# Kernel tuning notes

Measured on AMD Instinct MI355X. Metric: run time of the kernel, lower is better.

The kernel has to match this reference:

```python
import jax, jax.numpy as jnp
import numpy as np

HIDDEN = 64
NUM_FEATURES = 32
BATCH = 64
SEQ = 2048


def setup_inputs() -> dict:
    key = jax.random.key(0)
    k_t, k_m, k_wr, k_br, k_wi, k_bi = jax.random.split(key, 6)
    # strictly increasing event times via cumsum of positive gaps
    gaps = jax.random.uniform(k_t, (BATCH, SEQ), minval=0.01, maxval=1.0)
    times = jnp.cumsum(gaps, axis=1)  # [B, T]
    marks = jax.random.uniform(k_m, (BATCH, SEQ, NUM_FEATURES))
    batch = jnp.concatenate([times[:, :, None], marks], axis=2)  # [B, T, 1+F]
    d_in = NUM_FEATURES + HIDDEN
    W_rec = jax.random.normal(k_wr, (d_in, 7 * HIDDEN)) / jnp.sqrt(d_in)
    b_rec = jnp.zeros((7 * HIDDEN,))
    W_int = jax.random.normal(k_wi, (HIDDEN, NUM_FEATURES)) / jnp.sqrt(HIDDEN)
    b_int = jnp.zeros((NUM_FEATURES,))
    return {"batch": batch, "W_rec": W_rec, "b_rec": b_rec,
            "W_int": W_int, "b_int": b_int}


def _ctlstm_forward(batch, W_rec, b_rec, W_int, b_int):
    times = batch[:, :, 0]          # [B, T]
    marks = batch[:, :, 1:]         # [B, T, F]
    B, T, _ = marks.shape
    # inter-event time for step t is times[t+1]-times[t]; last step has no decay
    dt = jnp.diff(times, axis=1)                                   # [B, T-1]
    dt = jnp.concatenate([dt, jnp.zeros((B, 1), dt.dtype)], 1)     # [B, T]

    def step(carry, inputs):
        h, c_decay, c_bar = carry
        x_t, dt_t = inputs          # [B, F], [B]
        z = jnp.concatenate([x_t, h], axis=1) @ W_rec + b_rec      # [B, 7H]
        i, f, g, o, i_bar, f_bar, delta = jnp.split(z, 7, axis=1)
        i = jax.nn.sigmoid(i)
        f = jax.nn.sigmoid(f)
        g = jnp.tanh(g)
        o = jax.nn.sigmoid(o)
        i_bar = jax.nn.sigmoid(i_bar)
        f_bar = jax.nn.sigmoid(f_bar)
        delta = jax.nn.softplus(delta)
        c = f * c_decay + i * g                    # (5a)
        c_bar_n = f_bar * c_bar + i_bar * g        # (5b)
        c_decay_n = c_bar_n + (c - c_bar_n) * jnp.exp(-delta * dt_t[:, None])  # (7)
        h_n = o * jnp.tanh(c_decay_n)              # (4b)
        intensity = jax.nn.softplus(h_n @ W_int + b_int)  # (4a)
        return (h_n, c_decay_n, c_bar_n), (o, c, c_bar_n, delta, intensity)

    h0 = jnp.zeros((B, HIDDEN), batch.dtype)
    carry0 = (h0, h0, h0)
    xs = (jnp.swapaxes(marks, 0, 1), jnp.swapaxes(dt, 0, 1))  # time-major
    _, (o, c, c_bar, delta, intensity) = jax.lax.scan(step, carry0, xs)
    tm = lambda a: jnp.swapaxes(a, 0, 1)  # [T,B,*] -> [B,T,*]
    # intensity defined only for t < T-1 (last decay step is skipped in original)
    return (tm(o), tm(c), tm(c_bar), tm(delta), tm(intensity)[:, :-1, :])


def reference(batch, W_rec, b_rec, W_int, b_int):
    return _ctlstm_forward(batch, W_rec, b_rec, W_int, b_int)
```

## Files before the change

### kernel.cpp

```cpp
#include <hip/hip_runtime.h>
#include <hip/hip_bf16.h>

#define BATCHN 64
#define SEQ    2048
#define HID    64
#define NF     32
#define DIN    96
#define G7     448
#define CH     33
#define REC_T  256

using bf16 = __hip_bfloat16;

__device__ __forceinline__ float b2f(bf16 v) { return __bfloat162float(v); }

__device__ __forceinline__ float ldin(const void* p, size_t i, bool f32) {
    return f32 ? ((const float*)p)[i] : b2f(((const bf16*)p)[i]);
}

__device__ __forceinline__ float fast_rcp(float x) { return __builtin_amdgcn_rcpf(x); }
__device__ __forceinline__ float sigmoid_f(float x) {
    return fast_rcp(1.0f + __expf(-x));
}
__device__ __forceinline__ float tanh_f(float x) {
    float e = __expf(2.0f * x);
    return 1.0f - 2.0f * fast_rcp(e + 1.0f);
}
__device__ __forceinline__ float softplus_f(float x) {
    float e = __expf(-fabsf(x));
    return fmaxf(x, 0.0f) + __logf(1.0f + e);
}

__device__ __forceinline__ float rl(float v, int lane) {
    return __uint_as_float(__builtin_amdgcn_readlane(__float_as_uint(v), lane));
}

__global__ void detect_dtype(const void* batch, int* flag) {
    if (threadIdx.x != 0 || blockIdx.x != 0) return;
    const float* bf = (const float*)batch;
    bool mono = true;
    float prev = bf[0];
    if (!(prev > 0.004f && prev < 1.3f)) mono = false;
    for (int t = 1; t < 16 && mono; ++t) {
        float cur = bf[(size_t)t * CH];
        if (!(cur > prev && (cur - prev) < 1.3f)) mono = false;
        prev = cur;
    }
    *flag = mono ? 1 : 0;
}

__global__ __launch_bounds__(G7) void xproj_gemm(
    const void* __restrict__ batch, const void* __restrict__ W_rec,
    const void* __restrict__ b_rec, float* __restrict__ xz,
    const int* __restrict__ flag)
{
    const bool f32 = *flag != 0;
    const int tid = threadIdx.x;
    const size_t base = (size_t)blockIdx.x * 64;

    float wx[NF];
    if (f32) {
        const float* W = (const float*)W_rec;
#pragma unroll
        for (int k = 0; k < NF; ++k) wx[k] = W[(size_t)k * G7 + tid];
    } else {
        const bf16* W = (const bf16*)W_rec;
#pragma unroll
        for (int k = 0; k < NF; ++k) wx[k] = b2f(W[(size_t)k * G7 + tid]);
    }
    const float bias = ldin(b_rec, tid, f32);

    __shared__ __align__(16) float s_x[64][NF];
    for (int i = tid; i < 64 * NF; i += G7) {
        const int r = i >> 5, k = i & 31;
        s_x[r][k] = ldin(batch, (base + r) * CH + 1 + k, f32);
    }
    __syncthreads();

    for (int r = 0; r < 64; ++r) {
        const float4* xv = (const float4*)s_x[r];
        float a0 = 0.f, a1 = 0.f, a2 = 0.f, a3 = 0.f;
#pragma unroll
        for (int k4 = 0; k4 < NF / 4; ++k4) {
            float4 v = xv[k4];
            a0 = fmaf(v.x, wx[4 * k4 + 0], a0);
            a1 = fmaf(v.y, wx[4 * k4 + 1], a1);
            a2 = fmaf(v.z, wx[4 * k4 + 2], a2);
            a3 = fmaf(v.w, wx[4 * k4 + 3], a3);
        }
        xz[(base + r) * G7 + tid] = bias + ((a0 + a1) + (a2 + a3));
    }
}

__global__ __launch_bounds__(REC_T, 1) void ctlstm_rec_xz4(
    const void* __restrict__ batch, const void* __restrict__ W_rec,
    const float* __restrict__ xz, float* __restrict__ out,
    float* __restrict__ h_ws, const int* __restrict__ flag)
{
    const bool f32 = *flag != 0;
    const int tid  = threadIdx.x;
    const int wave = tid >> 6;
    const int lane = tid & 63;
    const int b    = blockIdx.x;
    const size_t bT = (size_t)b * SEQ;

    float* out_o  = out;
    float* out_c  = out + (size_t)BATCHN * SEQ * HID;
    float* out_cb = out + 2 * (size_t)BATCHN * SEQ * HID;
    float* out_dl = out + 3 * (size_t)BATCHN * SEQ * HID;

    __shared__ float s_act[2][G7];
    __shared__ float s_times[SEQ];

    const int c0 = tid;
    const int c1 = (wave < 3) ? tid + 256 : tid;

    float2 wh[HID];
    if (f32) {
        const float* W = (const float*)W_rec;
#pragma unroll
        for (int k = 0; k < HID; ++k) {
            wh[k].x = W[(size_t)(NF + k) * G7 + c0];
            wh[k].y = W[(size_t)(NF + k) * G7 + c1];
        }
    } else {
        const bf16* W = (const bf16*)W_rec;
#pragma unroll
        for (int k = 0; k < HID; ++k) {
            wh[k].x = b2f(W[(size_t)(NF + k) * G7 + c0]);
            wh[k].y = b2f(W[(size_t)(NF + k) * G7 + c1]);
        }
    }

    for (int i = tid; i < SEQ; i += REC_T)
        s_times[i] = ldin(batch, (bT + i) * CH, f32);

    float h_reg = 0.0f, c_decay = 0.0f, c_bar = 0.0f;

    float xa0 = xz[bT * G7 + c0];
    float xb0 = xz[bT * G7 + c1];
    float xa1 = xz[(bT + 1) * G7 + c0];
    float xb1 = xz[(bT + 1) * G7 + c1];
    __syncthreads();

    for (int t = 0; t < SEQ; ++t) {
        float xa2 = 0.0f, xb2 = 0.0f;
        if (t + 2 < SEQ) {
            xa2 = xz[(bT + t + 2) * G7 + c0];
            xb2 = xz[(bT + t + 2) * G7 + c1];
        }

        float a0x = 0.f, a1x = 0.f, a2x = 0.f, a3x = 0.f;
        float a0y = 0.f, a1y = 0.f, a2y = 0.f, a3y = 0.f;
#pragma unroll
        for (int k = 0; k < HID; k += 4) {
            const float h0 = rl(h_reg, k + 0);
            const float h1 = rl(h_reg, k + 1);
            const float h2 = rl(h_reg, k + 2);
            const float h3 = rl(h_reg, k + 3);
            a0x = fmaf(h0, wh[k + 0].x, a0x); a0y = fmaf(h0, wh[k + 0].y, a0y);
            a1x = fmaf(h1, wh[k + 1].x, a1x); a1y = fmaf(h1, wh[k + 1].y, a1y);
            a2x = fmaf(h2, wh[k + 2].x, a2x); a2y = fmaf(h2, wh[k + 2].y, a2y);
            a3x = fmaf(h3, wh[k + 3].x, a3x); a3y = fmaf(h3, wh[k + 3].y, a3y);
        }
        const float z0 = xa0 + ((a0x + a1x) + (a2x + a3x));
        const float z1 = xb0 + ((a0y + a1y) + (a2y + a3y));

        const float act0 = (wave == 2) ? tanh_f(z0) : sigmoid_f(z0);
        const float act1 = (wave == 2) ? softplus_f(z1) : sigmoid_f(z1);

        const int p = t & 1;
        s_act[p][c0] = act0;
        if (wave < 3) s_act[p][c1] = act1;

        asm volatile("s_waitcnt lgkmcnt(0)" ::: "memory");
        __builtin_amdgcn_s_barrier();
        __builtin_amdgcn_sched_barrier(0);

        const float ig = s_act[p][lane];
        const float fg = s_act[p][HID + lane];
        const float gg = s_act[p][2 * HID + lane];
        const float og = s_act[p][3 * HID + lane];
        const float ib = s_act[p][4 * HID + lane];
        const float fb = s_act[p][5 * HID + lane];
        const float dl = s_act[p][6 * HID + lane];
        const float c   = fg * c_decay + ig * gg;
        const float cbn = fb * c_bar + ib * gg;
        float dt = (t + 1 < SEQ) ? (s_times[t + 1] - s_times[t]) : 0.0f;
        dt = fmaxf(dt, 0.0f);
        const float cd = cbn + (c - cbn) * __expf(-dl * dt);
        const float h  = og * tanh_f(cd);
        c_decay = cd;
        c_bar   = cbn;
        h_reg   = h;

        const size_t idx = (bT + t) * HID + lane;
        if (wave == 0)      out_c[idx]  = c;
        else if (wave == 1) out_cb[idx] = cbn;
        else if (wave == 2) h_ws[idx]   = h;
        else                { out_o[idx] = og; out_dl[idx] = dl; }

        xa0 = xa1; xb0 = xb1; xa1 = xa2; xb1 = xb2;
    }
}

__global__ __launch_bounds__(G7, 2) void ctlstm_rec(
    const void* __restrict__ batch, const void* __restrict__ W_rec,
    const void* __restrict__ b_rec, float* __restrict__ out,
    float* __restrict__ h_ws, int use_ws, const int* __restrict__ flag)
{
    const bool f32 = flag ? (*flag != 0) : true;
    const int tid = threadIdx.x;
    const int b   = blockIdx.x;
    const size_t bT = (size_t)b * SEQ;

    float* out_o  = out;
    float* out_c  = out + (size_t)BATCHN * SEQ * HID;
    float* out_cb = out + 2 * (size_t)BATCHN * SEQ * HID;
    float* out_dl = out + 3 * (size_t)BATCHN * SEQ * HID;

    __shared__ __align__(16) float s_in[DIN];
    __shared__ float s_act[G7];
    __shared__ float s_times[SEQ];

    float wcol[DIN];
    if (f32) {
        const float* W = (const float*)W_rec;
#pragma unroll
        for (int k = 0; k < DIN; ++k) wcol[k] = W[(size_t)k * G7 + tid];
    } else {
        const bf16* W = (const bf16*)W_rec;
#pragma unroll
        for (int k = 0; k < DIN; ++k) wcol[k] = b2f(W[(size_t)k * G7 + tid]);
    }
    const float bias = ldin(b_rec, tid, f32);

    for (int i = tid; i < SEQ; i += G7)
        s_times[i] = ldin(batch, (bT + i) * CH, f32);

    if (tid >= NF && tid < DIN) s_in[tid] = 0.0f;
    float c_decay = 0.0f, c_bar = 0.0f;

    float xpref = 0.0f;
    if (tid < NF) xpref = ldin(batch, bT * CH + 1 + tid, f32);
    __syncthreads();

    const int gate = tid >> 6;
    const int lane = tid & 63;

    for (int t = 0; t < SEQ; ++t) {
        if (tid < NF) s_in[tid] = xpref;
        __syncthreads();

        const float4* sv = (const float4*)s_in;
        float a0 = 0.f, a1 = 0.f, a2 = 0.f, a3 = 0.f;
#pragma unroll
        for (int k4 = 0; k4 < DIN / 4; ++k4) {
            float4 v = sv[k4];
            a0 = fmaf(v.x, wcol[4 * k4 + 0], a0);
            a1 = fmaf(v.y, wcol[4 * k4 + 1], a1);
            a2 = fmaf(v.z, wcol[4 * k4 + 2], a2);
            a3 = fmaf(v.w, wcol[4 * k4 + 3], a3);
        }
        const float z = bias + ((a0 + a1) + (a2 + a3));

        float act;
        if (gate == 2)      act = tanh_f(z);
        else if (gate == 6) act = softplus_f(z);
        else                act = sigmoid_f(z);
        s_act[tid] = act;

        const size_t oidx = (bT + t) * HID + lane;
        if (gate == 3) out_o[oidx]  = act;
        if (gate == 6) out_dl[oidx] = act;
        __syncthreads();

        if (tid < HID) {
            const float ig = s_act[tid];
            const float fg = s_act[HID + tid];
            const float gg = s_act[2 * HID + tid];
            const float og = s_act[3 * HID + tid];
            const float ib = s_act[4 * HID + tid];
            const float fb = s_act[5 * HID + tid];
            const float dl = s_act[6 * HID + tid];
            const float c  = fg * c_decay + ig * gg;
            const float cb = fb * c_bar + ib * gg;
            float dt = (t + 1 < SEQ) ? (s_times[t + 1] - s_times[t]) : 0.0f;
            dt = fmaxf(dt, 0.0f);
            const float cd = cb + (c - cb) * __expf(-dl * dt);
            const float h  = og * tanh_f(cd);
            c_decay = cd;
            c_bar   = cb;
            s_in[NF + tid] = h;
            const size_t idx = (bT + t) * HID + tid;
            out_c[idx]  = c;
            out_cb[idx] = cb;
            if (use_ws) h_ws[idx] = h;
        }
        if (tid < NF && t + 1 < SEQ)
            xpref = ldin(batch, (bT + t + 1) * CH + 1 + tid, f32);
    }
}

__global__ __launch_bounds__(256) void intensity_ws(
    const float* __restrict__ h_ws, const void* __restrict__ W_int,
    const void* __restrict__ b_int, float* __restrict__ out_int,
    const int* __restrict__ flag)
{
    const bool f32 = flag ? (*flag != 0) : true;
    __shared__ float s_w[HID * NF];
    __shared__ float s_b[NF];
    const int tx = threadIdx.x, ty = threadIdx.y;
    const int lt = ty * 32 + tx;
    for (int k = lt; k < HID * NF; k += 256) s_w[k] = ldin(W_int, k, f32);
    if (lt < NF) s_b[lt] = ldin(b_int, lt, f32);
    __syncthreads();

    const int b = blockIdx.y;
    const int t = blockIdx.x * 8 + ty;
    if (t >= SEQ - 1) return;
    const float* hr = h_ws + ((size_t)b * SEQ + t) * HID;
    float acc = s_b[tx];
#pragma unroll
    for (int k = 0; k < HID; ++k) acc = fmaf(hr[k], s_w[k * NF + tx], acc);
    out_int[((size_t)b * (SEQ - 1) + t) * NF + tx] = softplus_f(acc);
}

__global__ __launch_bounds__(256) void intensity_rec(
    const void* __restrict__ batch, const float* __restrict__ out,
    const void* __restrict__ W_int, const void* __restrict__ b_int,
    float* __restrict__ out_int, const int* __restrict__ flag)
{
    const bool f32 = flag ? (*flag != 0) : true;
    __shared__ float s_w[HID * NF];
    __shared__ float s_b[NF];
    __shared__ float s_h[8][HID];
    const int tx = threadIdx.x, ty = threadIdx.y;
    const int lt = ty * 32 + tx;
    for (int k = lt; k < HID * NF; k += 256) s_w[k] = ldin(W_int, k, f32);
    if (lt < NF) s_b[lt] = ldin(b_int, lt, f32);

    const int b  = blockIdx.y;
    const int t0 = blockIdx.x * 8;
    const float* out_o  = out;
    const float* out_c  = out + (size_t)BATCHN * SEQ * HID;
    const float* out_cb = out + 2 * (size_t)BATCHN * SEQ * HID;
    const float* out_dl = out + 3 * (size_t)BATCHN * SEQ * HID;

#pragma unroll
    for (int r = 0; r < 2; ++r) {
        const int flat = lt + r * 256;
        const int row  = flat >> 6;
        const int k    = flat & 63;
        const int t    = t0 + row;
        if (t < SEQ - 1) {
            const size_t idx = ((size_t)b * SEQ + t) * HID + k;
            const float og = out_o[idx];
            const float c  = out_c[idx];
            const float cb = out_cb[idx];
            const float dl = out_dl[idx];
            const float t_a = ldin(batch, ((size_t)b * SEQ + t) * CH, f32);
            const float t_b = ldin(batch, ((size_t)b * SEQ + t + 1) * CH, f32);
            const float dt = fmaxf(t_b - t_a, 0.0f);
            const float cd = cb + (c - cb) * __expf(-dl * dt);
            s_h[row][k] = og * tanh_f(cd);
        }
    }
    __syncthreads();
    const int t = t0 + ty;
    if (t >= SEQ - 1) return;
    float acc = s_b[tx];
#pragma unroll
    for (int k = 0; k < HID; ++k) acc = fmaf(s_h[ty][k], s_w[k * NF + tx], acc);
    out_int[((size_t)b * (SEQ - 1) + t) * NF + tx] = softplus_f(acc);
}

extern "C" void kernel_launch(void* const* d_in, const int* in_sizes, int n_in,
                              void* d_out, int out_size, void* d_ws, size_t ws_size,
                              hipStream_t stream) {
    const void* batch = d_in[0];
    const void* W_rec = d_in[1];
    const void* b_rec = d_in[2];
    const void* W_int = d_in[3];
    const void* b_int = d_in[4];
    float* out = (float*)d_out;

    const size_t hb  = (size_t)BATCHN * SEQ * HID * sizeof(float);
    const size_t xzb = (size_t)BATCHN * SEQ * G7  * sizeof(float);
    int*   flag = (ws_size >= 4) ? (int*)d_ws : nullptr;
    float* h_ws = (float*)((char*)d_ws + 256);
    float* xz   = (float*)((char*)d_ws + 256 + hb);
    const int have_h  = (ws_size >= 256 + hb) ? 1 : 0;
    const int have_xz = (ws_size >= 256 + hb + xzb) ? 1 : 0;

    if (flag) detect_dtype<<<1, 64, 0, stream>>>(batch, flag);

    float* out_int = out + 4 * (size_t)BATCHN * SEQ * HID;

    if (have_xz) {
        xproj_gemm<<<(BATCHN * SEQ) / 64, G7, 0, stream>>>(batch, W_rec, b_rec, xz, flag);
        ctlstm_rec_xz4<<<BATCHN, REC_T, 0, stream>>>(batch, W_rec, xz, out, h_ws, flag);
        intensity_ws<<<dim3((SEQ - 1 + 7) / 8, BATCHN), dim3(32, 8), 0, stream>>>(
            h_ws, W_int, b_int, out_int, flag);
    } else if (have_h) {
        ctlstm_rec<<<BATCHN, G7, 0, stream>>>(batch, W_rec, b_rec, out, h_ws, 1, flag);
        intensity_ws<<<dim3((SEQ - 1 + 7) / 8, BATCHN), dim3(32, 8), 0, stream>>>(
            h_ws, W_int, b_int, out_int, flag);
    } else {
        ctlstm_rec<<<BATCHN, G7, 0, stream>>>(batch, W_rec, b_rec, out, h_ws, 0, flag);
        intensity_rec<<<dim3((SEQ - 1 + 7) / 8, BATCHN), dim3(32, 8), 0, stream>>>(
            batch, out, W_int, b_int, out_int, flag);
    }
}
```

Before: 1.788 ms.

## Move recurrent weights to LDS as packed bf16 and stream times from global

The recurrent kernel no longer keeps 128 fp32 weights per thread in registers. It packs the hidden-to-gate weights as bf16 pairs in LDS with a rotated layout to avoid bank conflicts, and reads them each step with 16-byte LDS loads. The shared times array is replaced by a two-ahead register prefetch of event times from global memory. This cuts VGPR pressure but adds LDS traffic on every step and rounds the fp32 weights to bf16, which costs some precision.

```diff
diff --git a/kernel.cpp b/kernel.cpp
--- a/kernel.cpp
+++ b/kernel.cpp
@@ -34,6 +34,14 @@
 __device__ __forceinline__ float rl(float v, int lane) {
     return __uint_as_float(__builtin_amdgcn_readlane(__float_as_uint(v), lane));
 }
+
+__device__ __forceinline__ unsigned int rne_hi16(float f) {
+    unsigned int u = __float_as_uint(f);
+    return (u + 0x7fffu + ((u >> 16) & 1u)) & 0xffff0000u;
+}
+
+#define HI16F(u) __uint_as_float((u) & 0xffff0000u)
+#define LO16F(u) __uint_as_float((u) << 16)
 
 __global__ void detect_dtype(const void* batch, int* flag) {
     if (threadIdx.x != 0 || blockIdx.x != 0) return;
@@ -92,7 +100,7 @@
     }
 }
 
-__global__ __launch_bounds__(REC_T, 1) void ctlstm_rec_xz4(
+__global__ __launch_bounds__(REC_T, 1) void ctlstm_rec_xzl(
     const void* __restrict__ batch, const void* __restrict__ W_rec,
     const float* __restrict__ xz, float* __restrict__ out,
     float* __restrict__ h_ws, const int* __restrict__ flag)
@@ -109,31 +117,50 @@
     float* out_cb = out + 2 * (size_t)BATCHN * SEQ * HID;
     float* out_dl = out + 3 * (size_t)BATCHN * SEQ * HID;
 
+    __shared__ unsigned int s_w[14336];
     __shared__ float s_act[2][G7];
-    __shared__ float s_times[SEQ];
 
     const int c0 = tid;
     const int c1 = (wave < 3) ? tid + 256 : tid;
 
-    float2 wh[HID];
+    const unsigned int mask  = (wave < 3) ? 15u : 7u;
+    unsigned int woff = (wave < 3) ? ((unsigned int)tid << 8)
+                                   : (49152u + ((unsigned int)lane << 7));
+
     if (f32) {
         const float* W = (const float*)W_rec;
-#pragma unroll
-        for (int k = 0; k < HID; ++k) {
-            wh[k].x = W[(size_t)(NF + k) * G7 + c0];
-            wh[k].y = W[(size_t)(NF + k) * G7 + c1];
+        for (int k2 = 0; k2 < 32; ++k2) {
+            unsigned int ue = rne_hi16(W[(size_t)(NF + 2 * k2) * G7 + c0]);
+            unsigned int uo = rne_hi16(W[(size_t)(NF + 2 * k2 + 1) * G7 + c0]);
+            unsigned int ch = (unsigned int)(k2 >> 2);
+            s_w[(woff >> 2) + (((ch + lane) & mask) << 2) + (k2 & 3)] = ue | (uo >> 16);
+            if (wave < 3) {
+                unsigned int ve = rne_hi16(W[(size_t)(NF + 2 * k2) * G7 + c1]);
+                unsigned int vo = rne_hi16(W[(size_t)(NF + 2 * k2 + 1) * G7 + c1]);
+                unsigned int cy = ch + 8u;
+                s_w[(woff >> 2) + (((cy + lane) & mask) << 2) + (k2 & 3)] = ve | (vo >> 16);
+            }
         }
     } else {
-        const bf16* W = (const bf16*)W_rec;
-#pragma unroll
-        for (int k = 0; k < HID; ++k) {
-            wh[k].x = b2f(W[(size_t)(NF + k) * G7 + c0]);
-            wh[k].y = b2f(W[(size_t)(NF + k) * G7 + c1]);
-        }
-    }
-
-    for (int i = tid; i < SEQ; i += REC_T)
-        s_times[i] = ldin(batch, (bT + i) * CH, f32);
+        const unsigned short* W = (const unsigned short*)W_rec;
+        for (int k2 = 0; k2 < 32; ++k2) {
+            unsigned int ue = ((unsigned int)W[(size_t)(NF + 2 * k2) * G7 + c0]) << 16;
+            unsigned int uo = (unsigned int)W[(size_t)(NF + 2 * k2 + 1) * G7 + c0];
+            unsigned int ch = (unsigned int)(k2 >> 2);
+            s_w[(woff >> 2) + (((ch + lane) & mask) << 2) + (k2 & 3)] = ue | uo;
+            if (wave < 3) {
+                unsigned int ve = ((unsigned int)W[(size_t)(NF + 2 * k2) * G7 + c1]) << 16;
+                unsigned int vo = (unsigned int)W[(size_t)(NF + 2 * k2 + 1) * G7 + c1];
+                unsigned int cy = ch + 8u;
+                s_w[(woff >> 2) + (((cy + lane) & mask) << 2) + (k2 & 3)] = ve | vo;
+            }
+        }
+    }
+
+#define O(i) const unsigned int o##i = ((((i) + (unsigned int)lane) & mask) << 4);
+    O(0) O(1) O(2) O(3) O(4) O(5) O(6) O(7)
+    O(8) O(9) O(10) O(11) O(12) O(13) O(14) O(15)
+#undef O
 
     float h_reg = 0.0f, c_decay = 0.0f, c_bar = 0.0f;
 
@@ -141,7 +168,21 @@
     float xb0 = xz[bT * G7 + c1];
     float xa1 = xz[(bT + 1) * G7 + c0];
     float xb1 = xz[(bT + 1) * G7 + c1];
+    float tmc = ldin(batch, (bT + 0) * CH, f32);
+    float tmn = ldin(batch, (bT + 1) * CH, f32);
     __syncthreads();
+
+#define LDQ(i) (*(const uint4*)((const char*)s_w + woff + o##i))
+#define CHUNK2(QX, QY, KB) { \
+    float hh; \
+    hh = rl(h_reg, (KB)+0); a0x = fmaf(hh, HI16F((QX).x), a0x); a0y = fmaf(hh, HI16F((QY).x), a0y); \
+    hh = rl(h_reg, (KB)+1); a1x = fmaf(hh, LO16F((QX).x), a1x); a1y = fmaf(hh, LO16F((QY).x), a1y); \
+    hh = rl(h_reg, (KB)+2); a0x = fmaf(hh, HI16F((QX).y), a0x); a0y = fmaf(hh, HI16F((QY).y), a0y); \
+    hh = rl(h_reg, (KB)+3); a1x = fmaf(hh, LO16F((QX).y), a1x); a1y = fmaf(hh, LO16F((QY).y), a1y); \
+    hh = rl(h_reg, (KB)+4); a0x = fmaf(hh, HI16F((QX).z), a0x); a0y = fmaf(hh, HI16F((QY).z), a0y); \
+    hh = rl(h_reg, (KB)+5); a1x = fmaf(hh, LO16F((QX).z), a1x); a1y = fmaf(hh, LO16F((QY).z), a1y); \
+    hh = rl(h_reg, (KB)+6); a0x = fmaf(hh, HI16F((QX).w), a0x); a0y = fmaf(hh, HI16F((QY).w), a0y); \
+    hh = rl(h_reg, (KB)+7); a1x = fmaf(hh, LO16F((QX).w), a1x); a1y = fmaf(hh, LO16F((QY).w), a1y); }
 
     for (int t = 0; t < SEQ; ++t) {
         float xa2 = 0.0f, xb2 = 0.0f;
@@ -149,22 +190,20 @@
             xa2 = xz[(bT + t + 2) * G7 + c0];
             xb2 = xz[(bT + t + 2) * G7 + c1];
         }
-
-        float a0x = 0.f, a1x = 0.f, a2x = 0.f, a3x = 0.f;
-        float a0y = 0.f, a1y = 0.f, a2y = 0.f, a3y = 0.f;
-#pragma unroll
-        for (int k = 0; k < HID; k += 4) {
-            const float h0 = rl(h_reg, k + 0);
-            const float h1 = rl(h_reg, k + 1);
-            const float h2 = rl(h_reg, k + 2);
-            const float h3 = rl(h_reg, k + 3);
-            a0x = fmaf(h0, wh[k + 0].x, a0x); a0y = fmaf(h0, wh[k + 0].y, a0y);
-            a1x = fmaf(h1, wh[k + 1].x, a1x); a1y = fmaf(h1, wh[k + 1].y, a1y);
-            a2x = fmaf(h2, wh[k + 2].x, a2x); a2y = fmaf(h2, wh[k + 2].y, a2y);
-            a3x = fmaf(h3, wh[k + 3].x, a3x); a3y = fmaf(h3, wh[k + 3].y, a3y);
-        }
-        const float z0 = xa0 + ((a0x + a1x) + (a2x + a3x));
-        const float z1 = xb0 + ((a0y + a1y) + (a2y + a3y));
+        const int tp2 = (t + 2 < SEQ) ? (t + 2) : (SEQ - 1);
+        const float tm2 = ldin(batch, (bT + tp2) * CH, f32);
+
+        asm volatile("" : "+v"(woff));
+        const uint4 q0 = LDQ(0),  q1 = LDQ(1),  q2 = LDQ(2),  q3 = LDQ(3);
+        const uint4 q4 = LDQ(4),  q5 = LDQ(5),  q6 = LDQ(6),  q7 = LDQ(7);
+        const uint4 r0 = LDQ(8),  r1 = LDQ(9),  r2 = LDQ(10), r3 = LDQ(11);
+        const uint4 r4 = LDQ(12), r5 = LDQ(13), r6 = LDQ(14), r7 = LDQ(15);
+
+        float a0x = 0.f, a1x = 0.f, a0y = 0.f, a1y = 0.f;
+        CHUNK2(q0, r0, 0)  CHUNK2(q1, r1, 8)  CHUNK2(q2, r2, 16) CHUNK2(q3, r3, 24)
+        CHUNK2(q4, r4, 32) CHUNK2(q5, r5, 40) CHUNK2(q6, r6, 48) CHUNK2(q7, r7, 56)
+        const float z0 = xa0 + (a0x + a1x);
+        const float z1 = xb0 + (a0y + a1y);
 
         const float act0 = (wave == 2) ? tanh_f(z0) : sigmoid_f(z0);
         const float act1 = (wave == 2) ? softplus_f(z1) : sigmoid_f(z1);
@@ -173,7 +212,8 @@
         s_act[p][c0] = act0;
         if (wave < 3) s_act[p][c1] = act1;
 
-        asm volatile("s_waitcnt lgkmcnt(0)" ::: "memory");
+        __builtin_amdgcn_sched_barrier(0);
+        asm volatile("s_waitcnt lgkmcnt(0)");
         __builtin_amdgcn_s_barrier();
         __builtin_amdgcn_sched_barrier(0);
 
@@ -186,8 +226,7 @@
         const float dl = s_act[p][6 * HID + lane];
         const float c   = fg * c_decay + ig * gg;
         const float cbn = fb * c_bar + ib * gg;
-        float dt = (t + 1 < SEQ) ? (s_times[t + 1] - s_times[t]) : 0.0f;
-        dt = fmaxf(dt, 0.0f);
+        const float dt  = fmaxf(tmn - tmc, 0.0f);
         const float cd = cbn + (c - cbn) * __expf(-dl * dt);
         const float h  = og * tanh_f(cd);
         c_decay = cd;
@@ -201,7 +240,10 @@
         else                { out_o[idx] = og; out_dl[idx] = dl; }
 
         xa0 = xa1; xb0 = xb1; xa1 = xa2; xb1 = xb2;
-    }
+        tmc = tmn; tmn = tm2;
+    }
+#undef LDQ
+#undef CHUNK2
 }
 
 __global__ __launch_bounds__(G7, 2) void ctlstm_rec(
@@ -399,7 +441,7 @@
 
     if (have_xz) {
         xproj_gemm<<<(BATCHN * SEQ) / 64, G7, 0, stream>>>(batch, W_rec, b_rec, xz, flag);
-        ctlstm_rec_xz4<<<BATCHN, REC_T, 0, stream>>>(batch, W_rec, xz, out, h_ws, flag);
+        ctlstm_rec_xzl<<<BATCHN, REC_T, 0, stream>>>(batch, W_rec, xz, out, h_ws, flag);
         intensity_ws<<<dim3((SEQ - 1 + 7) / 8, BATCHN), dim3(32, 8), 0, stream>>>(
             h_ws, W_int, b_int, out_int, flag);
     } else if (have_h) {
```

New measurement: 3.181 ms. 1.78x slower.

## Pack recurrent weights as bf16 pairs and reload them from cache each step

Applied to the files above, without the earlier changes.

Adds a prep kernel that rounds the hidden-to-gate weights to bf16 and packs pairs into a transposed buffer, placed temporarily in the intensity output region. The recurrent kernel no longer keeps 128 floats of weights in registers. It keeps 64 packed words and reloads them from global/L2 after each barrier, which lowers register pressure. This costs precision, because f32 weights are rounded to bf16, and it adds a per-step reload of 256 bytes per thread.

```diff
diff --git a/kernel.cpp b/kernel.cpp
--- a/kernel.cpp
+++ b/kernel.cpp
@@ -11,6 +11,7 @@
 #define REC_T  256
 
 using bf16 = __hip_bfloat16;
+typedef __attribute__((ext_vector_type(4))) unsigned int u32x4;
 
 __device__ __forceinline__ float b2f(bf16 v) { return __bfloat162float(v); }
 
@@ -34,6 +35,14 @@
 __device__ __forceinline__ float rl(float v, int lane) {
     return __uint_as_float(__builtin_amdgcn_readlane(__float_as_uint(v), lane));
 }
+
+__device__ __forceinline__ unsigned int rne_hi16(float f) {
+    unsigned int u = __float_as_uint(f);
+    return (u + 0x7fffu + ((u >> 16) & 1u)) & 0xffff0000u;
+}
+
+#define HI16F(u) __uint_as_float((u) & 0xffff0000u)
+#define LO16F(u) __uint_as_float((u) << 16)
 
 __global__ void detect_dtype(const void* batch, int* flag) {
     if (threadIdx.x != 0 || blockIdx.x != 0) return;
@@ -49,6 +58,26 @@
     *flag = mono ? 1 : 0;
 }
 
+__global__ __launch_bounds__(G7) void wt_prep(
+    const void* __restrict__ W_rec, unsigned int* __restrict__ Wt,
+    const int* __restrict__ flag)
+{
+    const bool f32 = *flag != 0;
+    const int p = blockIdx.x;
+    const int c = threadIdx.x;
+    unsigned int hi, lo;
+    if (f32) {
+        const float* W = (const float*)W_rec;
+        hi = rne_hi16(W[(size_t)(NF + 2 * p) * G7 + c]);
+        lo = rne_hi16(W[(size_t)(NF + 2 * p + 1) * G7 + c]) >> 16;
+    } else {
+        const unsigned short* W = (const unsigned short*)W_rec;
+        hi = ((unsigned int)W[(size_t)(NF + 2 * p) * G7 + c]) << 16;
+        lo = (unsigned int)W[(size_t)(NF + 2 * p + 1) * G7 + c];
+    }
+    Wt[(size_t)c * 32 + p] = hi | lo;
+}
+
 __global__ __launch_bounds__(G7) void xproj_gemm(
     const void* __restrict__ batch, const void* __restrict__ W_rec,
     const void* __restrict__ b_rec, float* __restrict__ xz,
@@ -92,8 +121,8 @@
     }
 }
 
-__global__ __launch_bounds__(REC_T, 1) void ctlstm_rec_xz4(
-    const void* __restrict__ batch, const void* __restrict__ W_rec,
+__global__ __launch_bounds__(REC_T, 1) void ctlstm_rec_xzt(
+    const void* __restrict__ batch, const unsigned int* __restrict__ Wt,
     const float* __restrict__ xz, float* __restrict__ out,
     float* __restrict__ h_ws, const int* __restrict__ flag)
 {
@@ -115,27 +144,18 @@
     const int c0 = tid;
     const int c1 = (wave < 3) ? tid + 256 : tid;
 
-    float2 wh[HID];
-    if (f32) {
-        const float* W = (const float*)W_rec;
-#pragma unroll
-        for (int k = 0; k < HID; ++k) {
-            wh[k].x = W[(size_t)(NF + k) * G7 + c0];
-            wh[k].y = W[(size_t)(NF + k) * G7 + c1];
-        }
-    } else {
-        const bf16* W = (const bf16*)W_rec;
-#pragma unroll
-        for (int k = 0; k < HID; ++k) {
-            wh[k].x = b2f(W[(size_t)(NF + k) * G7 + c0]);
-            wh[k].y = b2f(W[(size_t)(NF + k) * G7 + c1]);
-        }
-    }
+    const u32x4* wp0 = (const u32x4*)Wt + (size_t)c0 * 8;
+    const u32x4* wp1 = (const u32x4*)Wt + (size_t)c1 * 8;
 
     for (int i = tid; i < SEQ; i += REC_T)
         s_times[i] = ldin(batch, (bT + i) * CH, f32);
 
     float h_reg = 0.0f, c_decay = 0.0f, c_bar = 0.0f;
+
+    u32x4 q0 = wp0[0], q1 = wp0[1], q2 = wp0[2], q3 = wp0[3];
+    u32x4 q4 = wp0[4], q5 = wp0[5], q6 = wp0[6], q7 = wp0[7];
+    u32x4 r0 = wp1[0], r1 = wp1[1], r2 = wp1[2], r3 = wp1[3];
+    u32x4 r4 = wp1[4], r5 = wp1[5], r6 = wp1[6], r7 = wp1[7];
 
     float xa0 = xz[bT * G7 + c0];
     float xb0 = xz[bT * G7 + c1];
@@ -143,39 +163,49 @@
     float xb1 = xz[(bT + 1) * G7 + c1];
     __syncthreads();
 
+#define CHUNK2(QX, QY, KB) { \
+    float hh; unsigned int ux, uy; \
+    ux = (QX)[0]; uy = (QY)[0]; \
+    hh = rl(h_reg, (KB)+0); a0x = fmaf(hh, HI16F(ux), a0x); a0y = fmaf(hh, HI16F(uy), a0y); \
+    hh = rl(h_reg, (KB)+1); a1x = fmaf(hh, LO16F(ux), a1x); a1y = fmaf(hh, LO16F(uy), a1y); \
+    ux = (QX)[1]; uy = (QY)[1]; \
+    hh = rl(h_reg, (KB)+2); a0x = fmaf(hh, HI16F(ux), a0x); a0y = fmaf(hh, HI16F(uy), a0y); \
+    hh = rl(h_reg, (KB)+3); a1x = fmaf(hh, LO16F(ux), a1x); a1y = fmaf(hh, LO16F(uy), a1y); \
+    ux = (QX)[2]; uy = (QY)[2]; \
+    hh = rl(h_reg, (KB)+4); a0x = fmaf(hh, HI16F(ux), a0x); a0y = fmaf(hh, HI16F(uy), a0y); \
+    hh = rl(h_reg, (KB)+5); a1x = fmaf(hh, LO16F(ux), a1x); a1y = fmaf(hh, LO16F(uy), a1y); \
+    ux = (QX)[3]; uy = (QY)[3]; \
+    hh = rl(h_reg, (KB)+6); a0x = fmaf(hh, HI16F(ux), a0x); a0y = fmaf(hh, HI16F(uy), a0y); \
+    hh = rl(h_reg, (KB)+7); a1x = fmaf(hh, LO16F(ux), a1x); a1y = fmaf(hh, LO16F(uy), a1y); }
+
     for (int t = 0; t < SEQ; ++t) {
+        float a0x = 0.f, a1x = 0.f, a0y = 0.f, a1y = 0.f;
+        CHUNK2(q0, r0, 0)  CHUNK2(q1, r1, 8)  CHUNK2(q2, r2, 16) CHUNK2(q3, r3, 24)
+        CHUNK2(q4, r4, 32) CHUNK2(q5, r5, 40) CHUNK2(q6, r6, 48) CHUNK2(q7, r7, 56)
+        const float z0 = xa0 + (a0x + a1x);
+        const float z1 = xb0 + (a0y + a1y);
+
+        const float act0 = (wave == 2) ? tanh_f(z0) : sigmoid_f(z0);
+        const float act1 = (wave == 2) ? softplus_f(z1) : sigmoid_f(z1);
+
+        const int p = t & 1;
+        s_act[p][c0] = act0;
+        if (wave < 3) s_act[p][c1] = act1;
+
+        asm volatile("s_waitcnt lgkmcnt(0)" ::: "memory");
+        __builtin_amdgcn_s_barrier();
+        __builtin_amdgcn_sched_barrier(0);
+
+        q0 = wp0[0]; q1 = wp0[1]; q2 = wp0[2]; q3 = wp0[3];
+        q4 = wp0[4]; q5 = wp0[5]; q6 = wp0[6]; q7 = wp0[7];
+        r0 = wp1[0]; r1 = wp1[1]; r2 = wp1[2]; r3 = wp1[3];
+        r4 = wp1[4]; r5 = wp1[5]; r6 = wp1[6]; r7 = wp1[7];
+
         float xa2 = 0.0f, xb2 = 0.0f;
         if (t + 2 < SEQ) {
             xa2 = xz[(bT + t + 2) * G7 + c0];
             xb2 = xz[(bT + t + 2) * G7 + c1];
         }
-
-        float a0x = 0.f, a1x = 0.f, a2x = 0.f, a3x = 0.f;
-        float a0y = 0.f, a1y = 0.f, a2y = 0.f, a3y = 0.f;
-#pragma unroll
-        for (int k = 0; k < HID; k += 4) {
-            const float h0 = rl(h_reg, k + 0);
-            const float h1 = rl(h_reg, k + 1);
-            const float h2 = rl(h_reg, k + 2);
-            const float h3 = rl(h_reg, k + 3);
-            a0x = fmaf(h0, wh[k + 0].x, a0x); a0y = fmaf(h0, wh[k + 0].y, a0y);
-            a1x = fmaf(h1, wh[k + 1].x, a1x); a1y = fmaf(h1, wh[k + 1].y, a1y);
-            a2x = fmaf(h2, wh[k + 2].x, a2x); a2y = fmaf(h2, wh[k + 2].y, a2y);
-            a3x = fmaf(h3, wh[k + 3].x, a3x); a3y = fmaf(h3, wh[k + 3].y, a3y);
-        }
-        const float z0 = xa0 + ((a0x + a1x) + (a2x + a3x));
-        const float z1 = xb0 + ((a0y + a1y) + (a2y + a3y));
-
-        const float act0 = (wave == 2) ? tanh_f(z0) : sigmoid_f(z0);
-        const float act1 = (wave == 2) ? softplus_f(z1) : sigmoid_f(z1);
-
-        const int p = t & 1;
-        s_act[p][c0] = act0;
-        if (wave < 3) s_act[p][c1] = act1;
-
-        asm volatile("s_waitcnt lgkmcnt(0)" ::: "memory");
-        __builtin_amdgcn_s_barrier();
-        __builtin_amdgcn_sched_barrier(0);
 
         const float ig = s_act[p][lane];
         const float fg = s_act[p][HID + lane];
@@ -201,7 +231,10 @@
         else                { out_o[idx] = og; out_dl[idx] = dl; }
 
         xa0 = xa1; xb0 = xb1; xa1 = xa2; xb1 = xb2;
-    }
+
+        __builtin_amdgcn_sched_barrier(0);
+    }
+#undef CHUNK2
 }
 
 __global__ __launch_bounds__(G7, 2) void ctlstm_rec(
@@ -396,10 +429,12 @@
     if (flag) detect_dtype<<<1, 64, 0, stream>>>(batch, flag);
 
     float* out_int = out + 4 * (size_t)BATCHN * SEQ * HID;
+    unsigned int* Wt = (unsigned int*)out_int;
 
     if (have_xz) {
+        wt_prep<<<32, G7, 0, stream>>>(W_rec, Wt, flag);
         xproj_gemm<<<(BATCHN * SEQ) / 64, G7, 0, stream>>>(batch, W_rec, b_rec, xz, flag);
-        ctlstm_rec_xz4<<<BATCHN, REC_T, 0, stream>>>(batch, W_rec, xz, out, h_ws, flag);
+        ctlstm_rec_xzt<<<BATCHN, REC_T, 0, stream>>>(batch, Wt, xz, out, h_ws, flag);
         intensity_ws<<<dim3((SEQ - 1 + 7) / 8, BATCHN), dim3(32, 8), 0, stream>>>(
             h_ws, W_int, b_int, out_int, flag);
     } else if (have_h) {
```

Measured after the change: 5.400 ms. 202% more time.
